# Performance work log

Measured on AMD Instinct MI355X. Metric: run time of the kernel, lower is better.

## Reference

```python
import jax, jax.numpy as jnp
import numpy as np

N, W, K, C = 131072, 128, 1024, 4  # windows, window_size, codebook size, num residual codebooks


def setup_inputs() -> dict:
    key = jax.random.key(0)
    kx, kc = jax.random.split(key)
    X = jax.random.normal(kx, (N, W), dtype=jnp.float32)
    # nn.init.uniform_(weight, a=-1.0, b=1.0) for each codebook; same K for all stages -> stack [C, K, W]
    codebooks = jax.random.uniform(kc, (C, K, W), dtype=jnp.float32, minval=-1.0, maxval=1.0)
    return {"X": X, "codebooks": codebooks}


def reference(X, codebooks):
    """Residual quantization: per stage, euclidean cdist -> argmin -> gather min dist -> subtract codeword.

    Returns (idx [C, N] int32, dists [N, C] float32) matching (idx_list, torch.stack(dists_list, dim=1)).
    """

    def step(residual, cb):
        # squared euclidean distances: ||r||^2 - 2 r.c + ||c||^2  (same argmin as cdist; sqrt for min dist)
        r2 = jnp.sum(residual * residual, axis=-1, keepdims=True)          # [N, 1]
        c2 = jnp.sum(cb * cb, axis=-1)                                     # [K]
        d2 = r2 - 2.0 * jnp.einsum("nw,kw->nk", residual, cb) + c2         # [N, K]
        idx = jnp.argmin(d2, axis=-1)                                      # [N]
        min_d2 = jnp.take_along_axis(d2, idx[:, None], axis=-1)[:, 0]      # [N]
        min_dist = jnp.sqrt(jnp.maximum(min_d2, 0.0))
        residual = residual - cb[idx]                                      # codebook gather + subtract
        return residual, (idx.astype(jnp.int32), min_dist)

    _, (idxs, dists) = jax.lax.scan(step, X, codebooks)  # idxs [C, N], dists [C, N]
    return idxs, dists.T  # dists stacked along dim=1 -> [N, C]
```

## Files before the change

### kernel.cpp

```cpp
#include <hip/hip_runtime.h>
#include <math.h>

#define NRW 131072
#define W   128
#define K   1024
#define C   4
#define BN  64
#define NT  256

typedef _Float16 f16;
typedef _Float16 f16x8 __attribute__((ext_vector_type(8)));
typedef float    f32x4 __attribute__((ext_vector_type(4)));

__device__ __forceinline__ float fmulr(float a, float b){ return __fmul_rn(a,b); }
__device__ __forceinline__ float faddr(float a, float b){ return __fadd_rn(a,b); }
__device__ __forceinline__ float fsubr(float a, float b){ return __fsub_rn(a,b); }
__device__ __forceinline__ unsigned umin32(unsigned a, unsigned b){ return a < b ? a : b; }
__device__ __forceinline__ unsigned umax32(unsigned a, unsigned b){ return a > b ? a : b; }

__device__ float seq_sumsq_glb(const float* __restrict__ p){
    float a = 0.f;
    for (int w = 0; w < W; ++w){ const float v = p[w]; a = faddr(a, fmulr(v, v)); }
    return a;
}

__global__ __launch_bounds__(256) void c2_kernel(const float* __restrict__ CB,
                                                 float* __restrict__ c2g){
    const int kg = blockIdx.x * 256 + threadIdx.x;
    if (kg < C * K) c2g[kg] = seq_sumsq_glb(CB + (size_t)kg * W);
}

__global__ __launch_bounds__(256) void split_kernel(const float* __restrict__ CB,
                                                    f16* __restrict__ Bh){
    const int g  = blockIdx.x * 256 + threadIdx.x;
    const int s  = g >> 14, k = (g >> 4) & 1023, w8 = g & 15;
    const float* src = CB + ((size_t)(s * K + k)) * W + w8 * 8;
    const size_t off = ((((size_t)(s * 64 + (k >> 4)) * 4 + (w8 >> 2)) * 64)
                        + ((w8 & 3) * 16 + (k & 15))) * 8;
    f16x8 hv;
    #pragma unroll
    for (int j = 0; j < 8; ++j) hv[j] = (f16)src[j];
    *(f16x8*)(Bh + off) = hv;
}

#define DPP_TOP2(p1, p2, RCTL)                                                          \
    {                                                                                   \
        const unsigned q1 = (unsigned)__builtin_amdgcn_update_dpp((int)(p1), (int)(p1), \
                                                                  (RCTL), 0xF, 0xF, false); \
        const unsigned q2 = (unsigned)__builtin_amdgcn_update_dpp((int)(p2), (int)(p2), \
                                                                  (RCTL), 0xF, 0xF, false); \
        const unsigned t = umax32(p1, q1);                                              \
        p1 = umin32(p1, q1);                                                            \
        p2 = umin32(t, umin32(p2, q2));                                                 \
    }

#define PACK_INS(ACCV, C2V, KPK, S1, S2)                                                \
    {                                                                                   \
        const float sv = fmaf(-2.f, (ACCV), (C2V));                                     \
        const int   bb = __float_as_int(sv);                                            \
        const unsigned uu = ((unsigned)(bb ^ ((bb >> 31) | (int)0x80000000))            \
                             & 0xFFFFFC00u) | (KPK);                                    \
        const unsigned tmn = umin32((S1), uu);                                          \
        (S2) = umin32((S2), umax32((S1), uu));                                          \
        (S1) = tmn;                                                                     \
    }

#define INS4(VAL, C0, C1, C2, C3)                                                       \
    {                                                                                   \
        const unsigned v_ = (VAL);                                                      \
        if (v_ < (C3)){                                                                 \
            if (v_ < (C2)){ (C3) = (C2);                                                \
                if (v_ < (C1)){ (C2) = (C1);                                            \
                    if (v_ < (C0)){ (C1) = (C0); (C0) = v_; } else (C1) = v_;           \
                } else (C2) = v_;                                                       \
            } else (C3) = v_;                                                           \
        }                                                                               \
    }

__global__ __launch_bounds__(NT, 3) void rq15_kernel(
    const float* __restrict__ X, const float* __restrict__ CB,
    const float* __restrict__ c2g, const f16* __restrict__ BhG,
    float* __restrict__ out)
{
    __shared__ float Rt[BN][W + 4];
    __shared__ unsigned long long mslot[BN * 5];
    __shared__ int   cand[BN][4];
    __shared__ float dve[BN][4];
    __shared__ int   widx[BN];

    const int tid = threadIdx.x;
    const int wv  = tid >> 6;
    const int ln  = tid & 63;
    const int col = ln & 15;
    const int n0  = blockIdx.x * BN;

    for (int e = tid; e < BN * 32; e += NT){
        const int row = e >> 5, q = e & 31;
        const float4 v = *(const float4*)(X + (size_t)(n0 + row) * W + q * 4);
        *(float4*)(&Rt[row][q * 4]) = v;
    }

    for (int st = 0; st < C; ++st){
        const float*  cb  = CB + (size_t)st * K * W;
        const float4* cb4 = (const float4*)cb;
        const f16*    BhS = BhG + (size_t)st * 131072;

        __syncthreads();

        float c2reg[16];
        #pragma unroll
        for (int kbi = 0; kbi < 16; ++kbi)
            c2reg[kbi] = c2g[st * K + (((wv * 16 + kbi) << 4) + col)];

        f16x8 a[4][4];
        #pragma unroll
        for (int rbl = 0; rbl < 4; ++rbl){
            #pragma unroll
            for (int q = 0; q < 4; ++q){
                const int row = rbl * 16 + (ln & 15);
                const int w0  = q * 32 + ((ln >> 4) << 3);
                const float* rp = &Rt[row][w0];
                f16x8 h;
                #pragma unroll
                for (int j = 0; j < 8; ++j) h[j] = (f16)rp[j];
                a[rbl][q] = h;
            }
        }

        unsigned s1[4][4], s2[4][4];
        #pragma unroll
        for (int i = 0; i < 4; ++i)
            #pragma unroll
            for (int j = 0; j < 4; ++j){ s1[i][j] = 0xFFFFFFFFu; s2[i][j] = 0xFFFFFFFFu; }

        #pragma unroll 1
        for (int kbi = 0; kbi < 16; ++kbi){
            const int kb = wv * 16 + kbi;
            f16x8 bh0 = *(const f16x8*)(BhS + ((size_t)(kb * 4 + 0) * 64 + ln) * 8);
            f16x8 bh1 = *(const f16x8*)(BhS + ((size_t)(kb * 4 + 1) * 64 + ln) * 8);
            f16x8 bh2 = *(const f16x8*)(BhS + ((size_t)(kb * 4 + 2) * 64 + ln) * 8);
            f16x8 bh3 = *(const f16x8*)(BhS + ((size_t)(kb * 4 + 3) * 64 + ln) * 8);
            const unsigned kpk = (unsigned)((kb << 4) + col);
            const float    c2v = c2reg[kbi];

            #pragma unroll
            for (int rbl = 0; rbl < 4; ++rbl){
                f32x4 acc = {0.f, 0.f, 0.f, 0.f};
                acc = __builtin_amdgcn_mfma_f32_16x16x32_f16(a[rbl][0], bh0, acc, 0, 0, 0);
                acc = __builtin_amdgcn_mfma_f32_16x16x32_f16(a[rbl][1], bh1, acc, 0, 0, 0);
                acc = __builtin_amdgcn_mfma_f32_16x16x32_f16(a[rbl][2], bh2, acc, 0, 0, 0);
                acc = __builtin_amdgcn_mfma_f32_16x16x32_f16(a[rbl][3], bh3, acc, 0, 0, 0);
                PACK_INS(acc[0], c2v, kpk, s1[rbl][0], s2[rbl][0]);
                PACK_INS(acc[1], c2v, kpk, s1[rbl][1], s2[rbl][1]);
                PACK_INS(acc[2], c2v, kpk, s1[rbl][2], s2[rbl][2]);
                PACK_INS(acc[3], c2v, kpk, s1[rbl][3], s2[rbl][3]);
            }
        }

        #pragma unroll
        for (int rbl = 0; rbl < 4; ++rbl){
            #pragma unroll
            for (int rg = 0; rg < 4; ++rg){
                unsigned p1 = s1[rbl][rg], p2 = s2[rbl][rg];
                DPP_TOP2(p1, p2, 0x121)
                DPP_TOP2(p1, p2, 0x122)
                DPP_TOP2(p1, p2, 0x124)
                DPP_TOP2(p1, p2, 0x128)
                if (col == 0){
                    const int row = rbl * 16 + ((ln >> 4) << 2) + rg;
                    mslot[row * 5 + wv] =
                        ((unsigned long long)p2 << 32) | (unsigned long long)p1;
                }
            }
        }
        __syncthreads();

        if (tid < BN){
            unsigned c0 = 0xFFFFFFFFu, c1 = 0xFFFFFFFFu, c2m = 0xFFFFFFFFu, c3 = 0xFFFFFFFFu;
            #pragma unroll
            for (int i = 0; i < 4; ++i){
                const unsigned long long v = mslot[tid * 5 + i];
                const unsigned lo = (unsigned)v, hi = (unsigned)(v >> 32);
                INS4(lo, c0, c1, c2m, c3);
                INS4(hi, c0, c1, c2m, c3);
            }
            cand[tid][0] = (int)(c0 & 1023u);
            cand[tid][1] = (int)(c1 & 1023u);
            cand[tid][2] = (int)(c2m & 1023u);
            cand[tid][3] = (int)(c3 & 1023u);
        }
        __syncthreads();

        {
            const int row = tid >> 2, cd = tid & 3;
            const int k = cand[row][cd];
            const float* cw = cb + (size_t)k * W;
            float r2 = 0.f, dot = 0.f;
            for (int w = 0; w < W; ++w){
                const float rv = Rt[row][w];
                r2  = faddr(r2, fmulr(rv, rv));
                dot = __fmaf_rn(rv, cw[w], dot);
            }
            dve[row][cd] = faddr(fsubr(r2, faddr(dot, dot)), c2g[st * K + k]);
        }
        __syncthreads();

        if (tid < BN){
            float bd = dve[tid][0]; int bk = cand[tid][0];
            #pragma unroll
            for (int j = 1; j < 4; ++j){
                const float d = dve[tid][j]; const int k = cand[tid][j];
                if (d < bd || (d == bd && k < bk)){ bd = d; bk = k; }
            }
            widx[tid] = bk;
            out[(size_t)st * NRW + (n0 + tid)] = (float)bk;
            out[(size_t)C * NRW + (size_t)(n0 + tid) * C + st] = __fsqrt_rn(fmaxf(bd, 0.f));
        }
        __syncthreads();

        if (st < C - 1){
            for (int e = tid; e < BN * 32; e += NT){
                const int row = e >> 5, q = e & 31;
                const float4 v = cb4[(size_t)widx[row] * 32 + q];
                float* rp = &Rt[row][q * 4];
                rp[0] = fsubr(rp[0], v.x);
                rp[1] = fsubr(rp[1], v.y);
                rp[2] = fsubr(rp[2], v.z);
                rp[3] = fsubr(rp[3], v.w);
            }
        }
    }
}

extern "C" void kernel_launch(void* const* d_in, const int* in_sizes, int n_in,
                              void* d_out, int out_size, void* d_ws, size_t ws_size,
                              hipStream_t stream) {
    const float* X  = (const float*)d_in[0];
    const float* CB = (const float*)d_in[1];
    float* out = (float*)d_out;

    float* c2g = (float*)d_ws;
    f16*   Bh  = (f16*)((char*)d_ws + 16384);

    c2_kernel<<<dim3((C * K + 255) / 256), 256, 0, stream>>>(CB, c2g);
    split_kernel<<<dim3(C * K * 16 / 256), 256, 0, stream>>>(CB, Bh);
    rq15_kernel<<<dim3(NRW / BN), NT, 0, stream>>>(X, CB, c2g, Bh, out);
}
```

Baseline: 335.7 us.

## Split waves into 2x2 row/codeword tiles and simplify candidate packing with biased scores

```diff
diff --git a/kernel.cpp b/kernel.cpp
--- a/kernel.cpp
+++ b/kernel.cpp
@@ -11,6 +11,7 @@
 typedef _Float16 f16;
 typedef _Float16 f16x8 __attribute__((ext_vector_type(8)));
 typedef float    f32x4 __attribute__((ext_vector_type(4)));
+typedef unsigned long long u64;
 
 __device__ __forceinline__ float fmulr(float a, float b){ return __fmul_rn(a,b); }
 __device__ __forceinline__ float faddr(float a, float b){ return __fadd_rn(a,b); }
@@ -43,31 +44,18 @@
     *(f16x8*)(Bh + off) = hv;
 }
 
-#define DPP_TOP2(p1, p2, RCTL)                                                          \
+#define PACK_INS6(ACCV, C2B, KBIV, S1, S2)                                              \
     {                                                                                   \
-        const unsigned q1 = (unsigned)__builtin_amdgcn_update_dpp((int)(p1), (int)(p1), \
-                                                                  (RCTL), 0xF, 0xF, false); \
-        const unsigned q2 = (unsigned)__builtin_amdgcn_update_dpp((int)(p2), (int)(p2), \
-                                                                  (RCTL), 0xF, 0xF, false); \
-        const unsigned t = umax32(p1, q1);                                              \
-        p1 = umin32(p1, q1);                                                            \
-        p2 = umin32(t, umin32(p2, q2));                                                 \
-    }
-
-#define PACK_INS(ACCV, C2V, KPK, S1, S2)                                                \
+        const float sv = fmaf(-2.f, (ACCV), (C2B));                                     \
+        const unsigned uu = (__float_as_uint(sv) & 0xFFFFFFE0u) | (KBIV);               \
+        const unsigned mn = umin32((S1), uu);                                           \
+        (S2) = umin32((S2), umax32((S1), uu));                                          \
+        (S1) = mn;                                                                      \
+    }
+
+#define INS4_64(VAL, C0, C1, C2, C3)                                                    \
     {                                                                                   \
-        const float sv = fmaf(-2.f, (ACCV), (C2V));                                     \
-        const int   bb = __float_as_int(sv);                                            \
-        const unsigned uu = ((unsigned)(bb ^ ((bb >> 31) | (int)0x80000000))            \
-                             & 0xFFFFFC00u) | (KPK);                                    \
-        const unsigned tmn = umin32((S1), uu);                                          \
-        (S2) = umin32((S2), umax32((S1), uu));                                          \
-        (S1) = tmn;                                                                     \
-    }
-
-#define INS4(VAL, C0, C1, C2, C3)                                                       \
-    {                                                                                   \
-        const unsigned v_ = (VAL);                                                      \
+        const u64 v_ = (VAL);                                                           \
         if (v_ < (C3)){                                                                 \
             if (v_ < (C2)){ (C3) = (C2);                                                \
                 if (v_ < (C1)){ (C2) = (C1);                                            \
@@ -77,19 +65,22 @@
         }                                                                               \
     }
 
-__global__ __launch_bounds__(NT, 3) void rq15_kernel(
+__global__ __launch_bounds__(NT, 3) void rq17_kernel(
     const float* __restrict__ X, const float* __restrict__ CB,
     const float* __restrict__ c2g, const f16* __restrict__ BhG,
     float* __restrict__ out)
 {
     __shared__ float Rt[BN][W + 4];
-    __shared__ unsigned long long mslot[BN * 5];
+    __shared__ float c2l[K];
+    __shared__ u64   mslot[BN * 5];
     __shared__ int   cand[BN][4];
     __shared__ float dve[BN][4];
     __shared__ int   widx[BN];
 
     const int tid = threadIdx.x;
     const int wv  = tid >> 6;
+    const int rh  = wv >> 1;
+    const int kh  = wv & 1;
     const int ln  = tid & 63;
     const int col = ln & 15;
     const int n0  = blockIdx.x * BN;
@@ -107,82 +98,87 @@
 
         __syncthreads();
 
-        float c2reg[16];
+        for (int kk = tid; kk < K; kk += NT) c2l[kk] = c2g[st * K + kk] + 512.0f;
+        __syncthreads();
+
+        f16x8 a[2][4];
         #pragma unroll
-        for (int kbi = 0; kbi < 16; ++kbi)
-            c2reg[kbi] = c2g[st * K + (((wv * 16 + kbi) << 4) + col)];
-
-        f16x8 a[4][4];
-        #pragma unroll
-        for (int rbl = 0; rbl < 4; ++rbl){
+        for (int rbl = 0; rbl < 2; ++rbl){
             #pragma unroll
             for (int q = 0; q < 4; ++q){
-                const int row = rbl * 16 + (ln & 15);
+                const int row = rh * 32 + rbl * 16 + (ln & 15);
                 const int w0  = q * 32 + ((ln >> 4) << 3);
                 const float* rp = &Rt[row][w0];
                 f16x8 h;
                 #pragma unroll
                 for (int j = 0; j < 8; ++j) h[j] = (f16)rp[j];
                 a[rbl][q] = h;
-            }
-        }
-
-        unsigned s1[4][4], s2[4][4];
+                asm volatile("" : "+v"(a[rbl][q]));
+            }
+        }
+
+        unsigned s1[2][4], s2[2][4];
         #pragma unroll
-        for (int i = 0; i < 4; ++i)
+        for (int i = 0; i < 2; ++i)
             #pragma unroll
             for (int j = 0; j < 4; ++j){ s1[i][j] = 0xFFFFFFFFu; s2[i][j] = 0xFFFFFFFFu; }
 
-        #pragma unroll 1
-        for (int kbi = 0; kbi < 16; ++kbi){
-            const int kb = wv * 16 + kbi;
+        #pragma unroll 2
+        for (int kbi = 0; kbi < 32; ++kbi){
+            const int kb = kh * 32 + kbi;
             f16x8 bh0 = *(const f16x8*)(BhS + ((size_t)(kb * 4 + 0) * 64 + ln) * 8);
             f16x8 bh1 = *(const f16x8*)(BhS + ((size_t)(kb * 4 + 1) * 64 + ln) * 8);
             f16x8 bh2 = *(const f16x8*)(BhS + ((size_t)(kb * 4 + 2) * 64 + ln) * 8);
             f16x8 bh3 = *(const f16x8*)(BhS + ((size_t)(kb * 4 + 3) * 64 + ln) * 8);
-            const unsigned kpk = (unsigned)((kb << 4) + col);
-            const float    c2v = c2reg[kbi];
-
-            #pragma unroll
-            for (int rbl = 0; rbl < 4; ++rbl){
+            const float    c2b  = c2l[(kb << 4) + col];
+            const unsigned kbiv = (unsigned)kbi;
+
+            #pragma unroll
+            for (int rbl = 0; rbl < 2; ++rbl){
                 f32x4 acc = {0.f, 0.f, 0.f, 0.f};
                 acc = __builtin_amdgcn_mfma_f32_16x16x32_f16(a[rbl][0], bh0, acc, 0, 0, 0);
                 acc = __builtin_amdgcn_mfma_f32_16x16x32_f16(a[rbl][1], bh1, acc, 0, 0, 0);
                 acc = __builtin_amdgcn_mfma_f32_16x16x32_f16(a[rbl][2], bh2, acc, 0, 0, 0);
                 acc = __builtin_amdgcn_mfma_f32_16x16x32_f16(a[rbl][3], bh3, acc, 0, 0, 0);
-                PACK_INS(acc[0], c2v, kpk, s1[rbl][0], s2[rbl][0]);
-                PACK_INS(acc[1], c2v, kpk, s1[rbl][1], s2[rbl][1]);
-                PACK_INS(acc[2], c2v, kpk, s1[rbl][2], s2[rbl][2]);
-                PACK_INS(acc[3], c2v, kpk, s1[rbl][3], s2[rbl][3]);
-            }
-        }
-
+                PACK_INS6(acc[0], c2b, kbiv, s1[rbl][0], s2[rbl][0]);
+                PACK_INS6(acc[1], c2b, kbiv, s1[rbl][1], s2[rbl][1]);
+                PACK_INS6(acc[2], c2b, kbiv, s1[rbl][2], s2[rbl][2]);
+                PACK_INS6(acc[3], c2b, kbiv, s1[rbl][3], s2[rbl][3]);
+            }
+        }
+
+        const unsigned kbase = (unsigned)((kh * 32) << 4) + (unsigned)col;
         #pragma unroll
-        for (int rbl = 0; rbl < 4; ++rbl){
+        for (int rbl = 0; rbl < 2; ++rbl){
             #pragma unroll
             for (int rg = 0; rg < 4; ++rg){
-                unsigned p1 = s1[rbl][rg], p2 = s2[rbl][rg];
-                DPP_TOP2(p1, p2, 0x121)
-                DPP_TOP2(p1, p2, 0x122)
-                DPP_TOP2(p1, p2, 0x124)
-                DPP_TOP2(p1, p2, 0x128)
+                const unsigned v1 = s1[rbl][rg], v2 = s2[rbl][rg];
+                u64 a1 = ((u64)(v1 & 0xFFFFFFE0u) << 32) | (u64)(((v1 & 31u) << 4) + kbase);
+                u64 a2 = ((u64)(v2 & 0xFFFFFFE0u) << 32) | (u64)(((v2 & 31u) << 4) + kbase);
+                #pragma unroll
+                for (int m = 1; m <= 8; m <<= 1){
+                    const u64 o1 = (u64)__shfl_xor((long long)a1, m, 16);
+                    const u64 o2 = (u64)__shfl_xor((long long)a2, m, 16);
+                    const u64 t  = a1 > o1 ? a1 : o1;
+                    a1 = a1 < o1 ? a1 : o1;
+                    const u64 u2 = a2 < o2 ? a2 : o2;
+                    a2 = t < u2 ? t : u2;
+                }
                 if (col == 0){
-                    const int row = rbl * 16 + ((ln >> 4) << 2) + rg;
-                    mslot[row * 5 + wv] =
-                        ((unsigned long long)p2 << 32) | (unsigned long long)p1;
+                    const int row = rh * 32 + rbl * 16 + ((ln >> 4) << 2) + rg;
+                    mslot[row * 5 + kh * 2 + 0] = a1;
+                    mslot[row * 5 + kh * 2 + 1] = a2;
                 }
             }
         }
         __syncthreads();
 
         if (tid < BN){
-            unsigned c0 = 0xFFFFFFFFu, c1 = 0xFFFFFFFFu, c2m = 0xFFFFFFFFu, c3 = 0xFFFFFFFFu;
+            u64 c0 = ~0ull, c1 = ~0ull, c2m = ~0ull, c3 = ~0ull;
             #pragma unroll
             for (int i = 0; i < 4; ++i){
-                const unsigned long long v = mslot[tid * 5 + i];
-                const unsigned lo = (unsigned)v, hi = (unsigned)(v >> 32);
-                INS4(lo, c0, c1, c2m, c3);
-                INS4(hi, c0, c1, c2m, c3);
+                const u64 v = mslot[tid * 5 + i];
+                INS4_64(v, c0, c1, c2m, c3);
             }
             cand[tid][0] = (int)(c0 & 1023u);
             cand[tid][1] = (int)(c1 & 1023u);
@@ -244,5 +240,5 @@
 
     c2_kernel<<<dim3((C * K + 255) / 256), 256, 0, stream>>>(CB, c2g);
     split_kernel<<<dim3(C * K * 16 / 256), 256, 0, stream>>>(CB, Bh);
-    rq15_kernel<<<dim3(NRW / BN), NT, 0, stream>>>(X, CB, c2g, Bh, out);
-}
+    rq17_kernel<<<dim3(NRW / BN), NT, 0, stream>>>(X, CB, c2g, Bh, out);
+}
```

New measurement: 369.7 us. 1.1x slower.
